# Kernel optimization log

Hardware: AMD Instinct MI355X
Metric: run time of the kernel (lower is better)

The kernel has to match this reference:

```python
import jax, jax.numpy as jnp
import numpy as np
import math

Z, H, G, S = 4, 16, 4, 4096          # batch, q heads, kv groups, seq len
BLOCK = 32                            # compression block size
NB = S // BLOCK                       # number of compressed KV blocks (128)
DQK, DV = 128, 128                    # head dims


def setup_inputs() -> dict:
    key = jax.random.key(0)
    k1, k2, k3 = jax.random.split(key, 3)
    q = jax.random.normal(k1, (Z, H, S, DQK), jnp.float32)
    k_blocks = jax.random.normal(k2, (Z, G, NB, DQK), jnp.float32)
    v_blocks = jax.random.normal(k3, (Z, G, NB, DV), jnp.float32)
    # block j covers tokens [j*BLOCK, (j+1)*BLOCK), so it 'ends' at position (j+1)*BLOCK-1
    block_ends = (jnp.arange(1, NB + 1) * BLOCK - 1).astype(jnp.int32)
    return {"q": q, "k_blocks": k_blocks, "v_blocks": v_blocks, "block_ends": block_ends}


def reference(q, k_blocks, v_blocks, block_ends):
    """NSA compression attention fwd: block-end causal masking over compressed KV blocks.
    q: [Z,H,S,Dqk]; k_blocks/v_blocks: [Z,G,NB,D]; block_ends: [NB] int.
    Query at position m attends to compressed block j iff block_ends[j] <= m.
    Rows with no valid block output zeros (matching the kernel's l_i==0 path)."""
    Zb, Hb, Sb, Dq = q.shape
    Gb = k_blocks.shape[1]
    sm_scale = 1.0 / math.sqrt(Dq)
    # GQA: head h -> kv group h // (H // G)
    qg = (q * sm_scale).reshape(Zb, Gb, Hb // Gb, Sb, Dq)
    s = jnp.einsum('zghsd,zgnd->zghsn', qg, k_blocks)        # [Z,G,H/G,S,NB]
    pos = jnp.arange(Sb)
    mask = block_ends[None, :] <= pos[:, None]               # [S,NB]
    s_masked = jnp.where(mask, s, -jnp.inf)
    m = jnp.max(s_masked, axis=-1, keepdims=True)            # online-softmax max (M)
    m_safe = jnp.where(jnp.isfinite(m), m, 0.0)
    p = jnp.where(mask, jnp.exp(s_masked - jax.lax.stop_gradient(m_safe)), 0.0)
    l = jnp.sum(p, axis=-1, keepdims=True)                   # softmax denom (exp(L-M))
    o = jnp.einsum('zghsn,zgnv->zghsv', p, v_blocks)
    o = jnp.where(l > 0, o / jnp.where(l > 0, l, 1.0), 0.0)
    return o.reshape(Zb, Hb, Sb, -1)                         # [Z,H,S,Dv]
```

## Files before the change

kernel.cpp:

```cpp
#include <hip/hip_runtime.h>


#define Zc 4
#define Hc 16
#define Gc 4
#define Sc 4096
#define NBc 128
#define Dc 128
#define VST 136

typedef __attribute__((ext_vector_type(8))) short short8;
typedef __attribute__((ext_vector_type(4))) float float4v;

__device__ inline unsigned pk2bf(float a, float b) {
    union { float f; unsigned u; } x, y; x.f = a; y.f = b;
    return __builtin_amdgcn_perm(y.u + 0x8000u, x.u + 0x8000u, 0x07060302u);
}
__device__ inline short8 mkfrag(float4v f0, float4v f1) {
    union { short8 v; unsigned d[4]; } u;
    u.d[0] = pk2bf(f0[0], f0[1]);
    u.d[1] = pk2bf(f0[2], f0[3]);
    u.d[2] = pk2bf(f1[0], f1[1]);
    u.d[3] = pk2bf(f1[2], f1[3]);
    return u.v;
}

__global__ __launch_bounds__(256, 2)
void nsa_fwd(const float* __restrict__ q, const float* __restrict__ kb,
             const float* __restrict__ vb, float* __restrict__ out) {
    __shared__ __align__(16) short Ksh[NBc * VST];
    __shared__ __align__(16) short Vt[Dc * VST];

    const int bx   = blockIdx.x, m0 = bx * 128;
    const int h    = blockIdx.y, z = blockIdx.z, g = h >> 2;
    const int tid  = threadIdx.x;
    const int wq   = tid >> 6;
    const int lane = tid & 63;
    const int l16  = lane & 15;
    const int quad = lane >> 4;

    const int nvmax   = 4 * bx + 4;
    const int c_max   = (nvmax + 15) >> 4;
    const int kbi_max = (nvmax + 31) >> 5;

    const float* qbase = q + ((size_t)(z * Hc + h) * Sc + m0 + wq * 32) * Dc;
    float4v qraw[4][2][2];
    #pragma unroll
    for (int dk = 0; dk < 4; dk++)
        #pragma unroll
        for (int t = 0; t < 2; t++) {
            const float* s = qbase + (size_t)(t * 16 + l16) * Dc + dk * 32 + quad * 8;
            qraw[dk][t][0] = *(const float4v*)s;
            qraw[dk][t][1] = *(const float4v*)(s + 4);
        }

    const float* ksrc = kb + (size_t)(z * Gc + g) * NBc * Dc;
    #pragma unroll
    for (int it = 0; it < 8; it++) {
        int i = it * 256 + tid;
        int n = i >> 4, c8 = i & 15;
        const float* s = ksrc + (size_t)n * Dc + c8 * 8;
        float4v f0 = *(const float4v*)s, f1 = *(const float4v*)(s + 4);
        *(short8*)(Ksh + n * VST + c8 * 8) = mkfrag(f0, f1);
    }
    const float* vsrc = vb + (size_t)(z * Gc + g) * NBc * Dc;
    #pragma unroll
    for (int it = 0; it < 16; it++) {
        int i = it * 256 + tid;
        int c = i >> 7, n = i & 127;
        float4v f = *(const float4v*)(vsrc + (size_t)n * Dc + c * 4);
        #pragma unroll
        for (int k2 = 0; k2 < 4; k2++) {
            union { float f; unsigned u; } x; x.f = f[k2];
            Vt[(c * 4 + k2) * VST + n] = (short)((x.u + 0x8000u) >> 16);
        }
    }

    const float sm = 0.08838834764831845f;
    short8 qf[4][2];
    #pragma unroll
    for (int dk = 0; dk < 4; dk++)
        #pragma unroll
        for (int t = 0; t < 2; t++)
            qf[dk][t] = mkfrag(qraw[dk][t][0] * sm, qraw[dk][t][1] * sm);

    __syncthreads();

    float4v acc[8][2];
    #pragma unroll
    for (int c = 0; c < 8; c++)
        #pragma unroll
        for (int t = 0; t < 2; t++) acc[c][t] = (float4v)0.f;

    #pragma unroll
    for (int dk = 0; dk < 4; dk++)
        #pragma unroll
        for (int c = 0; c < 8; c++)
            if (c < c_max) {
                short8 a = *(const short8*)(Ksh + (c * 16 + l16) * VST + dk * 32 + quad * 8);
                acc[c][0] = __builtin_amdgcn_mfma_f32_16x16x32_bf16(a, qf[dk][0], acc[c][0], 0, 0, 0);
                acc[c][1] = __builtin_amdgcn_mfma_f32_16x16x32_bf16(a, qf[dk][1], acc[c][1], 0, 0, 0);
            }

    unsigned Ppk[8][2][2];
    #pragma unroll
    for (int c = 0; c < 8; c++)
        #pragma unroll
        for (int t = 0; t < 2; t++) { Ppk[c][t][0] = 0u; Ppk[c][t][1] = 0u; }

    #pragma unroll
    for (int t = 0; t < 2; t++) {
        const int mg = m0 + wq * 32 + t * 16 + l16;
        int nv = (mg + 1) >> 5; if (nv > NBc) nv = NBc;
        float mx = -1e30f;
        #pragma unroll
        for (int c = 0; c < 8; c++)
            if (c < c_max)
                #pragma unroll
                for (int r = 0; r < 4; r++) {
                    const int j = c * 16 + quad * 4 + r;
                    float s = acc[c][t][r];
                    s = (j < nv) ? s : -1e30f;
                    acc[c][t][r] = s;
                    mx = fmaxf(mx, s);
                }
        mx = fmaxf(mx, __shfl_xor(mx, 16, 64));
        mx = fmaxf(mx, __shfl_xor(mx, 32, 64));
        float ls = 0.f;
        #pragma unroll
        for (int c = 0; c < 8; c++)
            if (c < c_max)
                #pragma unroll
                for (int r = 0; r < 4; r++) {
                    float s = acc[c][t][r];
                    float p = (s > -1e29f) ? __expf(s - mx) : 0.f;
                    acc[c][t][r] = p;
                    ls += p;
                }
        ls += __shfl_xor(ls, 16, 64);
        ls += __shfl_xor(ls, 32, 64);
        const float inv = (ls > 0.f) ? 1.f / ls : 0.f;
        #pragma unroll
        for (int c = 0; c < 8; c++)
            if (c < c_max) {
                Ppk[c][t][0] = pk2bf(acc[c][t][0] * inv, acc[c][t][1] * inv);
                Ppk[c][t][1] = pk2bf(acc[c][t][2] * inv, acc[c][t][3] * inv);
            }
    }

    float4v oacc[8][2];
    #pragma unroll
    for (int c = 0; c < 8; c++)
        #pragma unroll
        for (int t = 0; t < 2; t++) oacc[c][t] = (float4v)0.f;

    const int s0 = (((2 * quad) & 3) << 4) | l16;
    const int s1 = (((2 * quad + 1) & 3) << 4) | l16;
    const bool hi = (quad >= 2);

    #pragma unroll
    for (int kbi = 0; kbi < 4; kbi++)
        if (kbi < kbi_max) {
            short8 ap[2];
            #pragma unroll
            for (int t = 0; t < 2; t++) {
                const int c1 = 2 * kbi;
                unsigned w0a = (unsigned)__shfl((int)Ppk[c1    ][t][0], s0, 64);
                unsigned w0b = (unsigned)__shfl((int)Ppk[c1 + 1][t][0], s0, 64);
                unsigned w1a = (unsigned)__shfl((int)Ppk[c1    ][t][1], s0, 64);
                unsigned w1b = (unsigned)__shfl((int)Ppk[c1 + 1][t][1], s0, 64);
                unsigned w2a = (unsigned)__shfl((int)Ppk[c1    ][t][0], s1, 64);
                unsigned w2b = (unsigned)__shfl((int)Ppk[c1 + 1][t][0], s1, 64);
                unsigned w3a = (unsigned)__shfl((int)Ppk[c1    ][t][1], s1, 64);
                unsigned w3b = (unsigned)__shfl((int)Ppk[c1 + 1][t][1], s1, 64);
                union { short8 v; unsigned d[4]; } u;
                u.d[0] = hi ? w0b : w0a;
                u.d[1] = hi ? w1b : w1a;
                u.d[2] = hi ? w2b : w2a;
                u.d[3] = hi ? w3b : w3a;
                ap[t] = u.v;
            }
            #pragma unroll
            for (int c = 0; c < 8; c++) {
                short8 bv = *(const short8*)(Vt + (c * 16 + l16) * VST + kbi * 32 + quad * 8);
                #pragma unroll
                for (int t = 0; t < 2; t++)
                    oacc[c][t] = __builtin_amdgcn_mfma_f32_16x16x32_bf16(ap[t], bv, oacc[c][t], 0, 0, 0);
            }
        }

    float* obase = out + ((size_t)(z * Hc + h) * Sc + m0 + wq * 32) * Dc;
    #pragma unroll
    for (int t = 0; t < 2; t++)
        #pragma unroll
        for (int rr = 0; rr < 4; rr++) {
            const int row = t * 16 + quad * 4 + rr;
            #pragma unroll
            for (int c = 0; c < 8; c++)
                obase[(size_t)row * Dc + c * 16 + l16] = oacc[c][t][rr];
        }
}

extern "C" void kernel_launch(void* const* d_in, const int* in_sizes, int n_in,
                              void* d_out, int out_size, void* d_ws, size_t ws_size,
                              hipStream_t stream) {
    const float* q  = (const float*)d_in[0];
    const float* kb = (const float*)d_in[1];
    const float* vb = (const float*)d_in[2];
    float* out = (float*)d_out;
    dim3 grid(Sc / 128, Hc, Zc);
    nsa_fwd<<<grid, dim3(256), 0, stream>>>(q, kb, vb, out);
}
```

Baseline: 251.7 us.

## Share one LDS buffer for K and transposed V, stage only causal-needed blocks

K and the transposed V now share a single LDS buffer. V is staged after the QK MFMAs, with a barrier in between, and that halves shared memory per workgroup; launch bounds go to four blocks per CU. K and V loads are also limited to the blocks the causal mask can reach, so early query tiles skip unneeded global reads. V staging is packed into 32-bit writes of two rows at a time. The trade-off is two extra barriers and a serialized V load after QK, plus tighter register budgets that could cause spills.

```diff
diff --git a/kernel.cpp b/kernel.cpp
--- a/kernel.cpp
+++ b/kernel.cpp
@@ -25,11 +25,10 @@
     return u.v;
 }
 
-__global__ __launch_bounds__(256, 2)
+__global__ __launch_bounds__(256, 4)
 void nsa_fwd(const float* __restrict__ q, const float* __restrict__ kb,
              const float* __restrict__ vb, float* __restrict__ out) {
-    __shared__ __align__(16) short Ksh[NBc * VST];
-    __shared__ __align__(16) short Vt[Dc * VST];
+    __shared__ __align__(16) short KV[NBc * VST];
 
     const int bx   = blockIdx.x, m0 = bx * 128;
     const int h    = blockIdx.y, z = blockIdx.z, g = h >> 2;
@@ -42,6 +41,7 @@
     const int nvmax   = 4 * bx + 4;
     const int c_max   = (nvmax + 15) >> 4;
     const int kbi_max = (nvmax + 31) >> 5;
+    const int nstage  = kbi_max << 5;
 
     const float* qbase = q + ((size_t)(z * Hc + h) * Sc + m0 + wq * 32) * Dc;
     float4v qraw[4][2][2];
@@ -56,25 +56,14 @@
 
     const float* ksrc = kb + (size_t)(z * Gc + g) * NBc * Dc;
     #pragma unroll
-    for (int it = 0; it < 8; it++) {
-        int i = it * 256 + tid;
-        int n = i >> 4, c8 = i & 15;
-        const float* s = ksrc + (size_t)n * Dc + c8 * 8;
-        float4v f0 = *(const float4v*)s, f1 = *(const float4v*)(s + 4);
-        *(short8*)(Ksh + n * VST + c8 * 8) = mkfrag(f0, f1);
-    }
-    const float* vsrc = vb + (size_t)(z * Gc + g) * NBc * Dc;
-    #pragma unroll
-    for (int it = 0; it < 16; it++) {
-        int i = it * 256 + tid;
-        int c = i >> 7, n = i & 127;
-        float4v f = *(const float4v*)(vsrc + (size_t)n * Dc + c * 4);
-        #pragma unroll
-        for (int k2 = 0; k2 < 4; k2++) {
-            union { float f; unsigned u; } x; x.f = f[k2];
-            Vt[(c * 4 + k2) * VST + n] = (short)((x.u + 0x8000u) >> 16);
-        }
-    }
+    for (int it = 0; it < 8; it++)
+        if (it < c_max) {
+            int i = it * 256 + tid;
+            int n = i >> 4, c8 = i & 15;
+            const float* s = ksrc + (size_t)n * Dc + c8 * 8;
+            float4v f0 = *(const float4v*)s, f1 = *(const float4v*)(s + 4);
+            *(short8*)(KV + n * VST + c8 * 8) = mkfrag(f0, f1);
+        }
 
     const float sm = 0.08838834764831845f;
     short8 qf[4][2];
@@ -97,10 +86,29 @@
         #pragma unroll
         for (int c = 0; c < 8; c++)
             if (c < c_max) {
-                short8 a = *(const short8*)(Ksh + (c * 16 + l16) * VST + dk * 32 + quad * 8);
+                short8 a = *(const short8*)(KV + (c * 16 + l16) * VST + dk * 32 + quad * 8);
                 acc[c][0] = __builtin_amdgcn_mfma_f32_16x16x32_bf16(a, qf[dk][0], acc[c][0], 0, 0, 0);
                 acc[c][1] = __builtin_amdgcn_mfma_f32_16x16x32_bf16(a, qf[dk][1], acc[c][1], 0, 0, 0);
             }
+
+    __syncthreads();
+
+    {
+        const float* vsrc = vb + (size_t)(z * Gc + g) * NBc * Dc;
+        const int np = tid & 63, n2 = np * 2;
+        const bool vact = (n2 < nstage);
+        #pragma unroll
+        for (int it = 0; it < 8; it++) {
+            const int c = it * 4 + wq;
+            if (vact) {
+                float4v fa = *(const float4v*)(vsrc + (size_t)n2 * Dc + c * 4);
+                float4v fb = *(const float4v*)(vsrc + (size_t)(n2 + 1) * Dc + c * 4);
+                #pragma unroll
+                for (int k2 = 0; k2 < 4; k2++)
+                    *(unsigned*)(KV + (c * 4 + k2) * VST + n2) = pk2bf(fa[k2], fb[k2]);
+            }
+        }
+    }
 
     unsigned Ppk[8][2][2];
     #pragma unroll
@@ -147,6 +155,8 @@
                 Ppk[c][t][1] = pk2bf(acc[c][t][2] * inv, acc[c][t][3] * inv);
             }
     }
+
+    __syncthreads();
 
     float4v oacc[8][2];
     #pragma unroll
@@ -182,7 +192,7 @@
             }
             #pragma unroll
             for (int c = 0; c < 8; c++) {
-                short8 bv = *(const short8*)(Vt + (c * 16 + l16) * VST + kbi * 32 + quad * 8);
+                short8 bv = *(const short8*)(KV + (c * 16 + l16) * VST + kbi * 32 + quad * 8);
                 #pragma unroll
                 for (int t = 0; t < 2; t++)
                     oacc[c][t] = __builtin_amdgcn_mfma_f32_16x16x32_bf16(ap[t], bv, oacc[c][t], 0, 0, 0);
```

Measured after the change: 257.4 us. +2.3%, slower.

## Share K/V staging across a KV group and pair causal tiles per wave

Applied to the files above, without the earlier changes.

Each 512-thread block now serves all four query heads of one KV group, so the bf16 K/V staging in shared memory is amortised over more work. Each wave processes two 32-row query tiles taken from opposite ends of the sequence, which balances the causal work per wave. The V transpose now writes packed pairs instead of single shorts. Costs are higher register pressure from launch_bounds(512,4), a serial two-iteration loop per wave, and fewer, larger blocks.

```diff
diff --git a/kernel.cpp b/kernel.cpp
--- a/kernel.cpp
+++ b/kernel.cpp
@@ -25,180 +25,186 @@
     return u.v;
 }
 
-__global__ __launch_bounds__(256, 2)
+__global__ __launch_bounds__(512, 4)
 void nsa_fwd(const float* __restrict__ q, const float* __restrict__ kb,
              const float* __restrict__ vb, float* __restrict__ out) {
     __shared__ __align__(16) short Ksh[NBc * VST];
     __shared__ __align__(16) short Vt[Dc * VST];
 
-    const int bx   = blockIdx.x, m0 = bx * 128;
-    const int h    = blockIdx.y, z = blockIdx.z, g = h >> 2;
+    const int wgp  = blockIdx.x;
+    const int g    = blockIdx.y, z = blockIdx.z;
     const int tid  = threadIdx.x;
     const int wq   = tid >> 6;
     const int lane = tid & 63;
     const int l16  = lane & 15;
     const int quad = lane >> 4;
 
-    const int nvmax   = 4 * bx + 4;
-    const int c_max   = (nvmax + 15) >> 4;
-    const int kbi_max = (nvmax + 31) >> 5;
-
-    const float* qbase = q + ((size_t)(z * Hc + h) * Sc + m0 + wq * 32) * Dc;
-    float4v qraw[4][2][2];
-    #pragma unroll
-    for (int dk = 0; dk < 4; dk++)
-        #pragma unroll
-        for (int t = 0; t < 2; t++) {
-            const float* s = qbase + (size_t)(t * 16 + l16) * Dc + dk * 32 + quad * 8;
-            qraw[dk][t][0] = *(const float4v*)s;
-            qraw[dk][t][1] = *(const float4v*)(s + 4);
-        }
+    const int W     = wgp * 8 + wq;
+    const int b     = W & 15;
+    const int h_loc = (W >> 4) & 3;
+    const int qq    = (W >> 6) & 3;
+    const int h     = g * 4 + h_loc;
 
     const float* ksrc = kb + (size_t)(z * Gc + g) * NBc * Dc;
     #pragma unroll
-    for (int it = 0; it < 8; it++) {
-        int i = it * 256 + tid;
+    for (int it = 0; it < 4; it++) {
+        int i = it * 512 + tid;
         int n = i >> 4, c8 = i & 15;
         const float* s = ksrc + (size_t)n * Dc + c8 * 8;
         float4v f0 = *(const float4v*)s, f1 = *(const float4v*)(s + 4);
         *(short8*)(Ksh + n * VST + c8 * 8) = mkfrag(f0, f1);
     }
-    const float* vsrc = vb + (size_t)(z * Gc + g) * NBc * Dc;
-    #pragma unroll
-    for (int it = 0; it < 16; it++) {
-        int i = it * 256 + tid;
-        int c = i >> 7, n = i & 127;
-        float4v f = *(const float4v*)(vsrc + (size_t)n * Dc + c * 4);
-        #pragma unroll
-        for (int k2 = 0; k2 < 4; k2++) {
-            union { float f; unsigned u; } x; x.f = f[k2];
-            Vt[(c * 4 + k2) * VST + n] = (short)((x.u + 0x8000u) >> 16);
+    {
+        const float* vsrc = vb + (size_t)(z * Gc + g) * NBc * Dc;
+        const int n2 = lane * 2;
+        #pragma unroll
+        for (int it = 0; it < 4; it++) {
+            const int c = it * 8 + wq;
+            float4v fa = *(const float4v*)(vsrc + (size_t)n2 * Dc + c * 4);
+            float4v fb = *(const float4v*)(vsrc + (size_t)(n2 + 1) * Dc + c * 4);
+            #pragma unroll
+            for (int k2 = 0; k2 < 4; k2++)
+                *(unsigned*)(Vt + (c * 4 + k2) * VST + n2) = pk2bf(fa[k2], fb[k2]);
         }
     }
 
+    __syncthreads();
+
     const float sm = 0.08838834764831845f;
-    short8 qf[4][2];
-    #pragma unroll
-    for (int dk = 0; dk < 4; dk++)
+
+    for (int si = 0; si < 2; si++) {
+        const int bx = si ? (31 - b) : b;
+        const int m0 = bx * 128 + qq * 32;
+        const int nvmax   = 4 * bx + qq + 1;
+        const int c_max   = (nvmax + 15) >> 4;
+        const int kbi_max = (nvmax + 31) >> 5;
+
+        const float* qbase = q + ((size_t)(z * Hc + h) * Sc + m0) * Dc;
+        short8 qf[4][2];
+        #pragma unroll
+        for (int dk = 0; dk < 4; dk++)
+            #pragma unroll
+            for (int t = 0; t < 2; t++) {
+                const float* s = qbase + (size_t)(t * 16 + l16) * Dc + dk * 32 + quad * 8;
+                float4v f0 = *(const float4v*)s;
+                float4v f1 = *(const float4v*)(s + 4);
+                qf[dk][t] = mkfrag(f0 * sm, f1 * sm);
+            }
+
+        float4v acc[8][2];
+        #pragma unroll
+        for (int c = 0; c < 8; c++)
+            #pragma unroll
+            for (int t = 0; t < 2; t++) acc[c][t] = (float4v)0.f;
+
+        #pragma unroll
+        for (int dk = 0; dk < 4; dk++)
+            #pragma unroll
+            for (int c = 0; c < 8; c++)
+                if (c < c_max) {
+                    short8 a = *(const short8*)(Ksh + (c * 16 + l16) * VST + dk * 32 + quad * 8);
+                    acc[c][0] = __builtin_amdgcn_mfma_f32_16x16x32_bf16(a, qf[dk][0], acc[c][0], 0, 0, 0);
+                    acc[c][1] = __builtin_amdgcn_mfma_f32_16x16x32_bf16(a, qf[dk][1], acc[c][1], 0, 0, 0);
+                }
+
+        unsigned Ppk[8][2][2];
+        #pragma unroll
+        for (int c = 0; c < 8; c++)
+            #pragma unroll
+            for (int t = 0; t < 2; t++) { Ppk[c][t][0] = 0u; Ppk[c][t][1] = 0u; }
+
+        #pragma unroll
+        for (int t = 0; t < 2; t++) {
+            const int mg = m0 + t * 16 + l16;
+            int nv = (mg + 1) >> 5; if (nv > NBc) nv = NBc;
+            float mx = -1e30f;
+            #pragma unroll
+            for (int c = 0; c < 8; c++)
+                if (c < c_max)
+                    #pragma unroll
+                    for (int r = 0; r < 4; r++) {
+                        const int j = c * 16 + quad * 4 + r;
+                        float s = acc[c][t][r];
+                        s = (j < nv) ? s : -1e30f;
+                        acc[c][t][r] = s;
+                        mx = fmaxf(mx, s);
+                    }
+            mx = fmaxf(mx, __shfl_xor(mx, 16, 64));
+            mx = fmaxf(mx, __shfl_xor(mx, 32, 64));
+            float ls = 0.f;
+            #pragma unroll
+            for (int c = 0; c < 8; c++)
+                if (c < c_max)
+                    #pragma unroll
+                    for (int r = 0; r < 4; r++) {
+                        float s = acc[c][t][r];
+                        float p = (s > -1e29f) ? __expf(s - mx) : 0.f;
+                        acc[c][t][r] = p;
+                        ls += p;
+                    }
+            ls += __shfl_xor(ls, 16, 64);
+            ls += __shfl_xor(ls, 32, 64);
+            const float inv = (ls > 0.f) ? 1.f / ls : 0.f;
+            #pragma unroll
+            for (int c = 0; c < 8; c++)
+                if (c < c_max) {
+                    Ppk[c][t][0] = pk2bf(acc[c][t][0] * inv, acc[c][t][1] * inv);
+                    Ppk[c][t][1] = pk2bf(acc[c][t][2] * inv, acc[c][t][3] * inv);
+                }
+        }
+
+        float4v oacc[8][2];
+        #pragma unroll
+        for (int c = 0; c < 8; c++)
+            #pragma unroll
+            for (int t = 0; t < 2; t++) oacc[c][t] = (float4v)0.f;
+
+        const int s0 = (((2 * quad) & 3) << 4) | l16;
+        const int s1 = (((2 * quad + 1) & 3) << 4) | l16;
+        const bool hi = (quad >= 2);
+
+        #pragma unroll
+        for (int kbi = 0; kbi < 4; kbi++)
+            if (kbi < kbi_max) {
+                short8 ap[2];
+                #pragma unroll
+                for (int t = 0; t < 2; t++) {
+                    const int c1 = 2 * kbi;
+                    unsigned w0a = (unsigned)__shfl((int)Ppk[c1    ][t][0], s0, 64);
+                    unsigned w0b = (unsigned)__shfl((int)Ppk[c1 + 1][t][0], s0, 64);
+                    unsigned w1a = (unsigned)__shfl((int)Ppk[c1    ][t][1], s0, 64);
+                    unsigned w1b = (unsigned)__shfl((int)Ppk[c1 + 1][t][1], s0, 64);
+                    unsigned w2a = (unsigned)__shfl((int)Ppk[c1    ][t][0], s1, 64);
+                    unsigned w2b = (unsigned)__shfl((int)Ppk[c1 + 1][t][0], s1, 64);
+                    unsigned w3a = (unsigned)__shfl((int)Ppk[c1    ][t][1], s1, 64);
+                    unsigned w3b = (unsigned)__shfl((int)Ppk[c1 + 1][t][1], s1, 64);
+                    union { short8 v; unsigned d[4]; } u;
+                    u.d[0] = hi ? w0b : w0a;
+                    u.d[1] = hi ? w1b : w1a;
+                    u.d[2] = hi ? w2b : w2a;
+                    u.d[3] = hi ? w3b : w3a;
+                    ap[t] = u.v;
+                }
+                #pragma unroll
+                for (int c = 0; c < 8; c++) {
+                    short8 bv = *(const short8*)(Vt + (c * 16 + l16) * VST + kbi * 32 + quad * 8);
+                    #pragma unroll
+                    for (int t = 0; t < 2; t++)
+                        oacc[c][t] = __builtin_amdgcn_mfma_f32_16x16x32_bf16(ap[t], bv, oacc[c][t], 0, 0, 0);
+                }
+            }
+
+        float* obase = out + ((size_t)(z * Hc + h) * Sc + m0) * Dc;
         #pragma unroll
         for (int t = 0; t < 2; t++)
-            qf[dk][t] = mkfrag(qraw[dk][t][0] * sm, qraw[dk][t][1] * sm);
-
-    __syncthreads();
-
-    float4v acc[8][2];
-    #pragma unroll
-    for (int c = 0; c < 8; c++)
-        #pragma unroll
-        for (int t = 0; t < 2; t++) acc[c][t] = (float4v)0.f;
-
-    #pragma unroll
-    for (int dk = 0; dk < 4; dk++)
-        #pragma unroll
-        for (int c = 0; c < 8; c++)
-            if (c < c_max) {
-                short8 a = *(const short8*)(Ksh + (c * 16 + l16) * VST + dk * 32 + quad * 8);
-                acc[c][0] = __builtin_amdgcn_mfma_f32_16x16x32_bf16(a, qf[dk][0], acc[c][0], 0, 0, 0);
-                acc[c][1] = __builtin_amdgcn_mfma_f32_16x16x32_bf16(a, qf[dk][1], acc[c][1], 0, 0, 0);
-            }
-
-    unsigned Ppk[8][2][2];
-    #pragma unroll
-    for (int c = 0; c < 8; c++)
-        #pragma unroll
-        for (int t = 0; t < 2; t++) { Ppk[c][t][0] = 0u; Ppk[c][t][1] = 0u; }
-
-    #pragma unroll
-    for (int t = 0; t < 2; t++) {
-        const int mg = m0 + wq * 32 + t * 16 + l16;
-        int nv = (mg + 1) >> 5; if (nv > NBc) nv = NBc;
-        float mx = -1e30f;
-        #pragma unroll
-        for (int c = 0; c < 8; c++)
-            if (c < c_max)
+            #pragma unroll
+            for (int rr = 0; rr < 4; rr++) {
+                const int row = t * 16 + quad * 4 + rr;
                 #pragma unroll
-                for (int r = 0; r < 4; r++) {
-                    const int j = c * 16 + quad * 4 + r;
-                    float s = acc[c][t][r];
-                    s = (j < nv) ? s : -1e30f;
-                    acc[c][t][r] = s;
-                    mx = fmaxf(mx, s);
-                }
-        mx = fmaxf(mx, __shfl_xor(mx, 16, 64));
-        mx = fmaxf(mx, __shfl_xor(mx, 32, 64));
-        float ls = 0.f;
-        #pragma unroll
-        for (int c = 0; c < 8; c++)
-            if (c < c_max)
-                #pragma unroll
-                for (int r = 0; r < 4; r++) {
-                    float s = acc[c][t][r];
-                    float p = (s > -1e29f) ? __expf(s - mx) : 0.f;
-                    acc[c][t][r] = p;
-                    ls += p;
-                }
-        ls += __shfl_xor(ls, 16, 64);
-        ls += __shfl_xor(ls, 32, 64);
-        const float inv = (ls > 0.f) ? 1.f / ls : 0.f;
-        #pragma unroll
-        for (int c = 0; c < 8; c++)
-            if (c < c_max) {
-                Ppk[c][t][0] = pk2bf(acc[c][t][0] * inv, acc[c][t][1] * inv);
-                Ppk[c][t][1] = pk2bf(acc[c][t][2] * inv, acc[c][t][3] * inv);
+                for (int c = 0; c < 8; c++)
+                    obase[(size_t)row * Dc + c * 16 + l16] = oacc[c][t][rr];
             }
     }
-
-    float4v oacc[8][2];
-    #pragma unroll
-    for (int c = 0; c < 8; c++)
-        #pragma unroll
-        for (int t = 0; t < 2; t++) oacc[c][t] = (float4v)0.f;
-
-    const int s0 = (((2 * quad) & 3) << 4) | l16;
-    const int s1 = (((2 * quad + 1) & 3) << 4) | l16;
-    const bool hi = (quad >= 2);
-
-    #pragma unroll
-    for (int kbi = 0; kbi < 4; kbi++)
-        if (kbi < kbi_max) {
-            short8 ap[2];
-            #pragma unroll
-            for (int t = 0; t < 2; t++) {
-                const int c1 = 2 * kbi;
-                unsigned w0a = (unsigned)__shfl((int)Ppk[c1    ][t][0], s0, 64);
-                unsigned w0b = (unsigned)__shfl((int)Ppk[c1 + 1][t][0], s0, 64);
-                unsigned w1a = (unsigned)__shfl((int)Ppk[c1    ][t][1], s0, 64);
-                unsigned w1b = (unsigned)__shfl((int)Ppk[c1 + 1][t][1], s0, 64);
-                unsigned w2a = (unsigned)__shfl((int)Ppk[c1    ][t][0], s1, 64);
-                unsigned w2b = (unsigned)__shfl((int)Ppk[c1 + 1][t][0], s1, 64);
-                unsigned w3a = (unsigned)__shfl((int)Ppk[c1    ][t][1], s1, 64);
-                unsigned w3b = (unsigned)__shfl((int)Ppk[c1 + 1][t][1], s1, 64);
-                union { short8 v; unsigned d[4]; } u;
-                u.d[0] = hi ? w0b : w0a;
-                u.d[1] = hi ? w1b : w1a;
-                u.d[2] = hi ? w2b : w2a;
-                u.d[3] = hi ? w3b : w3a;
-                ap[t] = u.v;
-            }
-            #pragma unroll
-            for (int c = 0; c < 8; c++) {
-                short8 bv = *(const short8*)(Vt + (c * 16 + l16) * VST + kbi * 32 + quad * 8);
-                #pragma unroll
-                for (int t = 0; t < 2; t++)
-                    oacc[c][t] = __builtin_amdgcn_mfma_f32_16x16x32_bf16(ap[t], bv, oacc[c][t], 0, 0, 0);
-            }
-        }
-
-    float* obase = out + ((size_t)(z * Hc + h) * Sc + m0 + wq * 32) * Dc;
-    #pragma unroll
-    for (int t = 0; t < 2; t++)
-        #pragma unroll
-        for (int rr = 0; rr < 4; rr++) {
-            const int row = t * 16 + quad * 4 + rr;
-            #pragma unroll
-            for (int c = 0; c < 8; c++)
-                obase[(size_t)row * Dc + c * 16 + l16] = oacc[c][t][rr];
-        }
 }
 
 extern "C" void kernel_launch(void* const* d_in, const int* in_sizes, int n_in,
@@ -208,6 +214,6 @@
     const float* kb = (const float*)d_in[1];
     const float* vb = (const float*)d_in[2];
     float* out = (float*)d_out;
-    dim3 grid(Sc / 128, Hc, Zc);
-    nsa_fwd<<<grid, dim3(256), 0, stream>>>(q, kb, vb, out);
-}
+    dim3 grid(32, Gc, Zc);
+    nsa_fwd<<<grid, dim3(512), 0, stream>>>(q, kb, vb, out);
+}
```

Result: slower. 312.5 us (+24.1%).
